# Kernel tuning notes

Hardware: AMD Instinct MI355X
Metric: run time of the kernel (lower is better)

## Reference

```python
import jax, jax.numpy as jnp
import numpy as np

LN_EPS = 1e-5
TOP_K = 2


def setup_inputs() -> dict:
    key = jax.random.key(0)
    ks = jax.random.split(key, 6)
    B, S, D, I, E = 4, 1024, 1024, 4096, 8
    return {
        "hidden_states": jax.random.normal(ks[0], (B, S, D), dtype=jnp.float32),
        "attention_mask": jnp.ones((B, S), dtype=jnp.float32),
        "gate_w": jax.random.normal(ks[1], (E, D), dtype=jnp.float32) * 0.02,
        "w1": jax.random.normal(ks[2], (E, D, I), dtype=jnp.float32) * 0.02,
        "b1": jnp.zeros((E, I), dtype=jnp.float32),
        "w2": jax.random.normal(ks[3], (E, I, D), dtype=jnp.float32) * 0.02,
        "b2": jnp.zeros((E, D), dtype=jnp.float32),
        "ln_gamma": jnp.ones((D,), dtype=jnp.float32),
        "ln_beta": jnp.zeros((D,), dtype=jnp.float32),
    }


def reference(hidden_states, attention_mask, gate_w, w1, b1, w2, b2, ln_gamma, ln_beta):
    B, S, D = hidden_states.shape
    E = gate_w.shape[0]
    h = hidden_states.reshape(-1, D).astype(jnp.float32)  # (T, D)

    # --- gate: softmax over experts, top-2, renormalize ---
    logits = h @ gate_w.T                                  # (T, E)
    probs = jax.nn.softmax(logits, axis=-1)
    rw, sel = jax.lax.top_k(probs, TOP_K)                  # (T, k), (T, k)
    rw = rw / jnp.sum(rw, axis=-1, keepdims=True)

    # per-token dense combine weights: (T, E), zero for non-selected experts
    onehot = jax.nn.one_hot(sel, E, dtype=rw.dtype)        # (T, k, E)
    w_te = jnp.einsum('tk,tke->te', rw, onehot)            # (T, E)

    # --- expert FFNs (dense over all experts; weights zero-out non-selected) ---
    mid = jax.nn.gelu(jnp.einsum('td,edi->eti', h, w1) + b1[:, None, :], approximate=False)
    eout = jnp.einsum('eti,eid->etd', mid, w2) + b2[:, None, :]  # (E, T, D)
    moe_out = jnp.einsum('etd,te->td', eout, w_te)         # (T, D)

    out = moe_out.reshape(B, S, D) * attention_mask[..., None]
    out = hidden_states + out

    # LayerNorm
    mu = jnp.mean(out, axis=-1, keepdims=True)
    var = jnp.var(out, axis=-1, keepdims=True)
    out = (out - mu) * jax.lax.rsqrt(var + LN_EPS) * ln_gamma + ln_beta

    # load balancing loss: mse(expert_usage, uniform)
    T = h.shape[0]
    usage = jnp.sum(onehot, axis=(0, 1)) / T               # (E,)
    aux_loss = jnp.mean((usage - 1.0 / E) ** 2)
    return out, aux_loss
```

## Files before the change

### kernel.cpp

```cpp
#include <hip/hip_runtime.h>
#include <hip/hip_bf16.h>
#include <math.h>

#define T_TOK 4096
#define D_DIM 1024
#define I_DIM 4096
#define E_EXP 8
#define MAX_TILES 48

typedef __attribute__((ext_vector_type(8))) short bf16x8;
typedef __attribute__((ext_vector_type(4))) float f32x4;

__device__ __forceinline__ unsigned short f2bf(float x) {
    unsigned int u = __float_as_uint(x);
    u += 0x7fffu + ((u >> 16) & 1u);
    return (unsigned short)(u >> 16);
}

__device__ __forceinline__ void glds16(const unsigned short* g, unsigned short* l) {
    __builtin_amdgcn_global_load_lds(
        (const __attribute__((address_space(1))) unsigned int*)g,
        (__attribute__((address_space(3))) unsigned int*)(unsigned int)(unsigned long long)(void*)l,
        16, 0, 0);
}

#define VMWAIT4 asm volatile("s_waitcnt vmcnt(4)" ::: "memory")
#define VMWAIT3 asm volatile("s_waitcnt vmcnt(3)" ::: "memory")
#define VMWAIT0 asm volatile("s_waitcnt vmcnt(0)" ::: "memory")

__device__ __forceinline__ void bar() {
    asm volatile("" ::: "memory");
    __builtin_amdgcn_s_barrier();
    asm volatile("" ::: "memory");
}

__global__ void gate_kernel(const float* __restrict__ h, const float* __restrict__ gw,
                            int* __restrict__ counts, int* __restrict__ sel,
                            float* __restrict__ wgt) {
    int t = blockIdx.x;
    int tid = threadIdx.x;
    float acc[E_EXP];
#pragma unroll
    for (int e = 0; e < E_EXP; e++) acc[e] = 0.f;
    const float* hr = h + (size_t)t * D_DIM;
    for (int d = tid; d < D_DIM; d += 256) {
        float hv = hr[d];
#pragma unroll
        for (int e = 0; e < E_EXP; e++) acc[e] += hv * gw[e * D_DIM + d];
    }
#pragma unroll
    for (int e = 0; e < E_EXP; e++)
        for (int off = 32; off > 0; off >>= 1) acc[e] += __shfl_down(acc[e], off, 64);
    __shared__ float red[4][E_EXP];
    int wave = tid >> 6, lane = tid & 63;
    if (lane == 0) {
#pragma unroll
        for (int e = 0; e < E_EXP; e++) red[wave][e] = acc[e];
    }
    __syncthreads();
    if (tid == 0) {
        float lg[E_EXP];
#pragma unroll
        for (int e = 0; e < E_EXP; e++) lg[e] = red[0][e] + red[1][e] + red[2][e] + red[3][e];
        float mx = lg[0];
#pragma unroll
        for (int e = 1; e < E_EXP; e++) mx = fmaxf(mx, lg[e]);
        float p[E_EXP];
#pragma unroll
        for (int e = 0; e < E_EXP; e++) p[e] = expf(lg[e] - mx);
        int i0 = 0; float b0 = p[0];
#pragma unroll
        for (int e = 1; e < E_EXP; e++) if (p[e] > b0) { b0 = p[e]; i0 = e; }
        int i1 = -1; float b1v = -1.f;
#pragma unroll
        for (int e = 0; e < E_EXP; e++) if (e != i0 && p[e] > b1v) { b1v = p[e]; i1 = e; }
        float den = b0 + b1v;
        sel[2 * t] = i0; sel[2 * t + 1] = i1;
        wgt[2 * t] = b0 / den; wgt[2 * t + 1] = b1v / den;
        atomicAdd(&counts[i0], 1);
        atomicAdd(&counts[i1], 1);
    }
}

__global__ void offsets_kernel(const int* __restrict__ counts, int* __restrict__ offs,
                               int* __restrict__ cursors, float* __restrict__ aux_out,
                               int* __restrict__ tile_e, int* __restrict__ tile_m,
                               int* __restrict__ ntiles) {
    if (blockIdx.x == 0 && threadIdx.x == 0) {
        int off = 0; float aux = 0.f; int nt = 0;
        for (int e = 0; e < E_EXP; e++) {
            offs[e] = off; off += counts[e]; cursors[e] = 0;
            float u = (float)counts[e] / (float)T_TOK;
            float d = u - 1.0f / (float)E_EXP;
            aux += d * d;
            for (int m0 = 0; m0 < counts[e]; m0 += 256) {
                tile_e[nt] = e; tile_m[nt] = m0; nt++;
            }
        }
        ntiles[0] = nt;
        aux_out[0] = aux / (float)E_EXP;
    }
}

__global__ void scatter_kernel(const int* __restrict__ sel, const float* __restrict__ wgt,
                               const int* __restrict__ offs, int* __restrict__ cursors,
                               int* __restrict__ tok_list, float* __restrict__ tok_w,
                               int* __restrict__ slot_of) {
    int t = blockIdx.x * 256 + threadIdx.x;
    if (t >= T_TOK) return;
#pragma unroll
    for (int k = 0; k < 2; k++) {
        int e = sel[2 * t + k];
        int pos = atomicAdd(&cursors[e], 1);
        int idx = offs[e] + pos;
        tok_list[idx] = t;
        tok_w[idx] = wgt[2 * t + k];
        slot_of[2 * t + k] = idx;
    }
}

__global__ void cvtH_kernel(const float* __restrict__ src, unsigned short* __restrict__ dst) {
    size_t i = ((size_t)blockIdx.x * 256 + threadIdx.x) * 8;
    float4 a = *(const float4*)(src + i);
    float4 b = *(const float4*)(src + i + 4);
    union { unsigned short u[8]; uint4 v; } o;
    o.u[0] = f2bf(a.x); o.u[1] = f2bf(a.y); o.u[2] = f2bf(a.z); o.u[3] = f2bf(a.w);
    o.u[4] = f2bf(b.x); o.u[5] = f2bf(b.y); o.u[6] = f2bf(b.z); o.u[7] = f2bf(b.w);
    *(uint4*)(dst + i) = o.v;
}

__global__ void transpose_cvt_kernel(const float* __restrict__ src, unsigned short* __restrict__ dst,
                                     int R, int C) {
    __shared__ float tile[32][33];
    int e = blockIdx.z;
    const float* s = src + (size_t)e * R * C;
    unsigned short* d = dst + (size_t)e * R * C;
    int c0 = blockIdx.x * 32, r0 = blockIdx.y * 32;
    int tx = threadIdx.x, ty = threadIdx.y;
#pragma unroll
    for (int j = 0; j < 4; j++)
        tile[ty + 8 * j][tx] = s[(size_t)(r0 + ty + 8 * j) * C + c0 + tx];
    __syncthreads();
#pragma unroll
    for (int j = 0; j < 4; j++)
        d[(size_t)(c0 + ty + 8 * j) * R + r0 + tx] = f2bf(tile[tx][ty + 8 * j]);
}

template <int MODE>
__launch_bounds__(512, 2)
__global__ void moe_gemm_kernel(const unsigned short* __restrict__ Abase,
                                const unsigned short* __restrict__ Bt,
                                const float* __restrict__ bias,
                                const int* __restrict__ counts, const int* __restrict__ offs,
                                const int* __restrict__ tile_e, const int* __restrict__ tile_m,
                                const int* __restrict__ ntiles,
                                const int* __restrict__ tok_list, const float* __restrict__ tok_w,
                                unsigned short* __restrict__ midout, float* __restrict__ slotbuf) {
    constexpr int K  = (MODE == 0) ? D_DIM : I_DIM;
    constexpr int N  = (MODE == 0) ? I_DIM : D_DIM;
    constexpr int BN = (MODE == 0) ? 256 : 128;
    constexpr int NJ = BN / 64;
    constexpr int SB = BN / 128;
    constexpr int NT = K / 32;

    __shared__ __align__(16) unsigned short lA[4][256 * 32];
    __shared__ __align__(16) unsigned short lB[4][BN * 32];

    const int nwg  = gridDim.x * gridDim.y;
    const int flat = blockIdx.y * gridDim.x + blockIdx.x;
    const int q8 = nwg >> 3, r8 = nwg & 7;
    const int xcd = flat & 7, pos = flat >> 3;
    const int id2 = (xcd < r8 ? xcd * (q8 + 1) : r8 * (q8 + 1) + (xcd - r8) * q8) + pos;
    const int tix = id2 / gridDim.y;
    const int nb  = id2 % gridDim.y;
    if (tix >= ntiles[0]) return;

    const int e   = tile_e[tix];
    const int m0  = tile_m[tix];
    const int Ne  = counts[e];
    const int seg = offs[e];
    const int n0  = nb * BN;

    const int tid  = threadIdx.x;
    const int w    = tid >> 6;
    const int lane = tid & 63;
    const int quad = lane >> 4;
    const int l15  = lane & 15;
    const int wm   = (w >> 2) * 128;
    const int wn   = (w & 3) * (NJ * 16);

    const int lrow = lane >> 2;
    const int lcol = (lane & 3) * 8;
    const unsigned short* gA0;
    const unsigned short* gA1;
    {
        int mr0 = m0 + w * 32 + lrow;
        int mr1 = mr0 + 16;
        int c0 = (mr0 < Ne) ? mr0 : 0;
        int c1 = (mr1 < Ne) ? mr1 : 0;
        size_t r0, r1;
        if (MODE == 0) { r0 = (size_t)tok_list[seg + c0] * K; r1 = (size_t)tok_list[seg + c1] * K; }
        else           { r0 = (size_t)(seg + c0) * K;         r1 = (size_t)(seg + c1) * K; }
        gA0 = Abase + r0 + lcol;
        gA1 = Abase + r1 + lcol;
    }
    const unsigned short* Bte = Bt + (size_t)e * N * K;
    const unsigned short* gB0 = Bte + (size_t)(n0 + w * (16 * SB) + lrow) * K + lcol;
    const unsigned short* gB1 = gB0 + (size_t)16 * K;

    auto ISSUE = [&](int kt2) {
        const int b2  = kt2 & 3;
        const int off = kt2 * 32;
        glds16(gA0 + off, &lA[b2][w * 1024]);
        glds16(gA1 + off, &lA[b2][w * 1024 + 512]);
        glds16(gB0 + off, &lB[b2][w * (SB * 512)]);
        if constexpr (MODE == 0) glds16(gB1 + off, &lB[b2][w * 1024 + 512]);
    };

    f32x4 acc[8][NJ];
#pragma unroll
    for (int a = 0; a < 8; a++)
#pragma unroll
        for (int j = 0; j < NJ; j++) acc[a][j] = (f32x4){0.f, 0.f, 0.f, 0.f};

    const int sc = quad * 8;

    auto TILE = [&](int kt2) {
        const unsigned short* LA = lA[kt2 & 3];
        const unsigned short* LB = lB[kt2 & 3];
        bf16x8 bv[NJ];
#pragma unroll
        for (int j = 0; j < NJ; j++)
            bv[j] = *(const bf16x8*)&LB[(wn + j * 16 + l15) * 32 + sc];
#pragma unroll
        for (int pm = 0; pm < 2; pm++) {
            bf16x8 av[4];
#pragma unroll
            for (int ii = 0; ii < 4; ii++)
                av[ii] = *(const bf16x8*)&LA[(wm + pm * 64 + ii * 16 + l15) * 32 + sc];
            __builtin_amdgcn_s_setprio(1);
#pragma unroll
            for (int ii = 0; ii < 4; ii++)
#pragma unroll
                for (int j = 0; j < NJ; j++)
                    acc[pm * 4 + ii][j] = __builtin_amdgcn_mfma_f32_16x16x32_bf16(
                        av[ii], bv[j], acc[pm * 4 + ii][j], 0, 0, 0);
            __builtin_amdgcn_s_setprio(0);
        }
    };

    ISSUE(0);
    ISSUE(1);

    for (int kt = 0; kt < NT; kt += 2) {
        if constexpr (MODE == 0) { VMWAIT4; } else { VMWAIT3; }
        bar();
        if (kt + 2 < NT) ISSUE(kt + 2);
        TILE(kt);
        if (kt + 3 < NT) {
            if constexpr (MODE == 0) { VMWAIT4; } else { VMWAIT3; }
        } else {
            VMWAIT0;
        }
        bar();
        if (kt + 3 < NT) ISSUE(kt + 3);
        TILE(kt + 1);
    }

    const float* be = bias + (size_t)e * N;
#pragma unroll
    for (int a = 0; a < 8; a++) {
        const int mbase = m0 + wm + (a >> 2) * 64 + (a & 3) * 16 + quad * 4;
#pragma unroll
        for (int j = 0; j < NJ; j++) {
            const int n = n0 + wn + j * 16 + l15;
            const float bvl = be[n];
#pragma unroll
            for (int r = 0; r < 4; r++) {
                const int m = mbase + r;
                if (m < Ne) {
                    float v = acc[a][j][r] + bvl;
                    if (MODE == 0) {
                        v = 0.5f * v * (1.0f + erff(v * 0.70710678118654752f));
                        midout[(size_t)(seg + m) * N + n] = f2bf(v);
                    } else {
                        slotbuf[(size_t)(seg + m) * N + n] = tok_w[seg + m] * v;
                    }
                }
            }
        }
    }
}

__global__ void ln_kernel(const float* __restrict__ hs, const float* __restrict__ mask,
                          const float* __restrict__ slotbuf, const int* __restrict__ slot_of,
                          const float* __restrict__ gamma, const float* __restrict__ beta,
                          float* __restrict__ outp) {
    int t = blockIdx.x, tid = threadIdx.x;
    int s0 = slot_of[2 * t], s1 = slot_of[2 * t + 1];
    float mk = mask[t];
    const float4* hr = (const float4*)(hs + (size_t)t * D_DIM);
    const float4* p0 = (const float4*)(slotbuf + (size_t)s0 * D_DIM);
    const float4* p1 = (const float4*)(slotbuf + (size_t)s1 * D_DIM);
    float4 hv = hr[tid], a = p0[tid], b = p1[tid];
    float x0 = hv.x + mk * (a.x + b.x);
    float x1 = hv.y + mk * (a.y + b.y);
    float x2 = hv.z + mk * (a.z + b.z);
    float x3 = hv.w + mk * (a.w + b.w);
    float sum = x0 + x1 + x2 + x3;
    float sq = x0 * x0 + x1 * x1 + x2 * x2 + x3 * x3;
    for (int off = 32; off > 0; off >>= 1) {
        sum += __shfl_down(sum, off, 64);
        sq += __shfl_down(sq, off, 64);
    }
    __shared__ float rsum[4], rsq[4];
    __shared__ float mu_s, rstd_s;
    int wave = tid >> 6, lane = tid & 63;
    if (lane == 0) { rsum[wave] = sum; rsq[wave] = sq; }
    __syncthreads();
    if (tid == 0) {
        float s = rsum[0] + rsum[1] + rsum[2] + rsum[3];
        float q = rsq[0] + rsq[1] + rsq[2] + rsq[3];
        float mu = s / (float)D_DIM;
        float var = q / (float)D_DIM - mu * mu;
        mu_s = mu; rstd_s = rsqrtf(var + 1e-5f);
    }
    __syncthreads();
    float mu = mu_s, rstd = rstd_s;
    const float4* g4 = (const float4*)gamma;
    const float4* b4 = (const float4*)beta;
    float4 g = g4[tid], bb = b4[tid];
    float4 o;
    o.x = (x0 - mu) * rstd * g.x + bb.x;
    o.y = (x1 - mu) * rstd * g.y + bb.y;
    o.z = (x2 - mu) * rstd * g.z + bb.z;
    o.w = (x3 - mu) * rstd * g.w + bb.w;
    ((float4*)(outp + (size_t)t * D_DIM))[tid] = o;
}

extern "C" void kernel_launch(void* const* d_in, const int* in_sizes, int n_in,
                              void* d_out, int out_size, void* d_ws, size_t ws_size,
                              hipStream_t stream) {
    const float* hs    = (const float*)d_in[0];
    const float* mask  = (const float*)d_in[1];
    const float* gw    = (const float*)d_in[2];
    const float* w1    = (const float*)d_in[3];
    const float* b1    = (const float*)d_in[4];
    const float* w2    = (const float*)d_in[5];
    const float* b2    = (const float*)d_in[6];
    const float* gamma = (const float*)d_in[7];
    const float* beta  = (const float*)d_in[8];
    float* out = (float*)d_out;

    char* ws = (char*)d_ws;
    int*   counts   = (int*)(ws + 0);
    int*   cursors  = (int*)(ws + 64);
    int*   offs     = (int*)(ws + 128);
    int*   ntiles   = (int*)(ws + 256);
    int*   tile_e   = (int*)(ws + 512);
    int*   tile_m   = (int*)(ws + 1024);
    int*   sel      = (int*)(ws + 4096);
    float* wgt      = (float*)(ws + 4096 + 1 * 32768);
    int*   slot_of  = (int*)(ws + 4096 + 2 * 32768);
    int*   tok_list = (int*)(ws + 4096 + 3 * 32768);
    float* tok_w    = (float*)(ws + 4096 + 4 * 32768);
    unsigned short* Hbf = (unsigned short*)(ws + (1ull << 20));
    unsigned short* W1t = (unsigned short*)(ws + (9ull << 20));
    unsigned short* W2t = (unsigned short*)(ws + (73ull << 20));
    unsigned short* mid = (unsigned short*)(ws + (137ull << 20));
    float* slotbuf      = (float*)(ws + (201ull << 20));

    hipMemsetAsync(counts, 0, 64, stream);
    gate_kernel<<<T_TOK, 256, 0, stream>>>(hs, gw, counts, sel, wgt);
    offsets_kernel<<<1, 64, 0, stream>>>(counts, offs, cursors, out + (size_t)T_TOK * D_DIM,
                                         tile_e, tile_m, ntiles);
    scatter_kernel<<<T_TOK / 256, 256, 0, stream>>>(sel, wgt, offs, cursors, tok_list, tok_w, slot_of);
    cvtH_kernel<<<(T_TOK * D_DIM / 8) / 256, 256, 0, stream>>>(hs, Hbf);
    transpose_cvt_kernel<<<dim3(I_DIM / 32, D_DIM / 32, E_EXP), dim3(32, 8), 0, stream>>>(w1, W1t, D_DIM, I_DIM);
    transpose_cvt_kernel<<<dim3(D_DIM / 32, I_DIM / 32, E_EXP), dim3(32, 8), 0, stream>>>(w2, W2t, I_DIM, D_DIM);
    moe_gemm_kernel<0><<<dim3(MAX_TILES, I_DIM / 256), 512, 0, stream>>>(
        Hbf, W1t, b1, counts, offs, tile_e, tile_m, ntiles, tok_list, tok_w, mid, nullptr);
    moe_gemm_kernel<1><<<dim3(MAX_TILES, D_DIM / 128), 512, 0, stream>>>(
        mid, W2t, b2, counts, offs, tile_e, tile_m, ntiles, tok_list, tok_w, nullptr, slotbuf);
    ln_kernel<<<T_TOK, 256, 0, stream>>>(hs, mask, slotbuf, slot_of, gamma, beta, out);
}
```

Before: 817.4 us.

## Restructure MoE GEMM pipeline with swizzled LDS, split A/B loads, uniform 256 N-tile

Rewrites the grouped GEMM main loop into a finer-grained schedule: A and B global-to-LDS loads are issued separately and interleaved between half-tile MFMA batches, with explicit lgkmcnt waits and barriers around each MFMA group. Adds an XOR swizzle on the LDS column offset to cut bank conflicts on fragment reads. The down-projection GEMM now uses a 256-wide N tile like the up-projection, and MAX_TILES shrinks from 48 to 40 to trim the grid. This brings more barriers per k-step, fewer workgroups for the second GEMM, and a tile cap that could be too small for unbalanced routing.

```diff
diff --git a/kernel.cpp b/kernel.cpp
--- a/kernel.cpp
+++ b/kernel.cpp
@@ -6,7 +6,7 @@
 #define D_DIM 1024
 #define I_DIM 4096
 #define E_EXP 8
-#define MAX_TILES 48
+#define MAX_TILES 40
 
 typedef __attribute__((ext_vector_type(8))) short bf16x8;
 typedef __attribute__((ext_vector_type(4))) float f32x4;
@@ -25,13 +25,11 @@
 }
 
 #define VMWAIT4 asm volatile("s_waitcnt vmcnt(4)" ::: "memory")
-#define VMWAIT3 asm volatile("s_waitcnt vmcnt(3)" ::: "memory")
 #define VMWAIT0 asm volatile("s_waitcnt vmcnt(0)" ::: "memory")
+#define LGKM0   asm volatile("s_waitcnt lgkmcnt(0)" ::: "memory")
 
 __device__ __forceinline__ void bar() {
-    asm volatile("" ::: "memory");
     __builtin_amdgcn_s_barrier();
-    asm volatile("" ::: "memory");
 }
 
 __global__ void gate_kernel(const float* __restrict__ h, const float* __restrict__ gw,
@@ -158,13 +156,10 @@
                                 unsigned short* __restrict__ midout, float* __restrict__ slotbuf) {
     constexpr int K  = (MODE == 0) ? D_DIM : I_DIM;
     constexpr int N  = (MODE == 0) ? I_DIM : D_DIM;
-    constexpr int BN = (MODE == 0) ? 256 : 128;
-    constexpr int NJ = BN / 64;
-    constexpr int SB = BN / 128;
     constexpr int NT = K / 32;
 
     __shared__ __align__(16) unsigned short lA[4][256 * 32];
-    __shared__ __align__(16) unsigned short lB[4][BN * 32];
+    __shared__ __align__(16) unsigned short lB[4][256 * 32];
 
     const int nwg  = gridDim.x * gridDim.y;
     const int flat = blockIdx.y * gridDim.x + blockIdx.x;
@@ -179,7 +174,7 @@
     const int m0  = tile_m[tix];
     const int Ne  = counts[e];
     const int seg = offs[e];
-    const int n0  = nb * BN;
+    const int n0  = nb * 256;
 
     const int tid  = threadIdx.x;
     const int w    = tid >> 6;
@@ -187,12 +182,13 @@
     const int quad = lane >> 4;
     const int l15  = lane & 15;
     const int wm   = (w >> 2) * 128;
-    const int wn   = (w & 3) * (NJ * 16);
+    const int wn   = (w & 3) * 64;
 
     const int lrow = lane >> 2;
-    const int lcol = (lane & 3) * 8;
-    const unsigned short* gA0;
-    const unsigned short* gA1;
+    const int scol = (((lane & 3) ^ ((lane >> 3) & 3)) & 3) * 8;
+    const int rs   = (((quad ^ ((l15 >> 1) & 3)) & 3) * 8);
+
+    const unsigned short *gA0, *gA1;
     {
         int mr0 = m0 + w * 32 + lrow;
         int mr1 = mr0 + 16;
@@ -201,70 +197,85 @@
         size_t r0, r1;
         if (MODE == 0) { r0 = (size_t)tok_list[seg + c0] * K; r1 = (size_t)tok_list[seg + c1] * K; }
         else           { r0 = (size_t)(seg + c0) * K;         r1 = (size_t)(seg + c1) * K; }
-        gA0 = Abase + r0 + lcol;
-        gA1 = Abase + r1 + lcol;
+        gA0 = Abase + r0 + scol;
+        gA1 = Abase + r1 + scol;
     }
     const unsigned short* Bte = Bt + (size_t)e * N * K;
-    const unsigned short* gB0 = Bte + (size_t)(n0 + w * (16 * SB) + lrow) * K + lcol;
+    const unsigned short* gB0 = Bte + (size_t)(n0 + w * 32 + lrow) * K + scol;
     const unsigned short* gB1 = gB0 + (size_t)16 * K;
 
-    auto ISSUE = [&](int kt2) {
-        const int b2  = kt2 & 3;
-        const int off = kt2 * 32;
-        glds16(gA0 + off, &lA[b2][w * 1024]);
-        glds16(gA1 + off, &lA[b2][w * 1024 + 512]);
-        glds16(gB0 + off, &lB[b2][w * (SB * 512)]);
-        if constexpr (MODE == 0) glds16(gB1 + off, &lB[b2][w * 1024 + 512]);
-    };
-
-    f32x4 acc[8][NJ];
+    auto ISSUE_A = [&](int t) {
+        const int b = t & 3, off = t * 32;
+        glds16(gA0 + off, &lA[b][w * 1024]);
+        glds16(gA1 + off, &lA[b][w * 1024 + 512]);
+    };
+    auto ISSUE_B = [&](int t) {
+        const int b = t & 3, off = t * 32;
+        glds16(gB0 + off, &lB[b][w * 1024]);
+        glds16(gB1 + off, &lB[b][w * 1024 + 512]);
+    };
+
+    f32x4 acc[8][4];
 #pragma unroll
     for (int a = 0; a < 8; a++)
 #pragma unroll
-        for (int j = 0; j < NJ; j++) acc[a][j] = (f32x4){0.f, 0.f, 0.f, 0.f};
-
-    const int sc = quad * 8;
-
-    auto TILE = [&](int kt2) {
-        const unsigned short* LA = lA[kt2 & 3];
-        const unsigned short* LB = lB[kt2 & 3];
-        bf16x8 bv[NJ];
-#pragma unroll
-        for (int j = 0; j < NJ; j++)
-            bv[j] = *(const bf16x8*)&LB[(wn + j * 16 + l15) * 32 + sc];
-#pragma unroll
-        for (int pm = 0; pm < 2; pm++) {
-            bf16x8 av[4];
-#pragma unroll
-            for (int ii = 0; ii < 4; ii++)
-                av[ii] = *(const bf16x8*)&LA[(wm + pm * 64 + ii * 16 + l15) * 32 + sc];
-            __builtin_amdgcn_s_setprio(1);
-#pragma unroll
-            for (int ii = 0; ii < 4; ii++)
-#pragma unroll
-                for (int j = 0; j < NJ; j++)
-                    acc[pm * 4 + ii][j] = __builtin_amdgcn_mfma_f32_16x16x32_bf16(
-                        av[ii], bv[j], acc[pm * 4 + ii][j], 0, 0, 0);
-            __builtin_amdgcn_s_setprio(0);
-        }
-    };
-
-    ISSUE(0);
-    ISSUE(1);
-
-    for (int kt = 0; kt < NT; kt += 2) {
-        if constexpr (MODE == 0) { VMWAIT4; } else { VMWAIT3; }
-        bar();
-        if (kt + 2 < NT) ISSUE(kt + 2);
-        TILE(kt);
-        if (kt + 3 < NT) {
-            if constexpr (MODE == 0) { VMWAIT4; } else { VMWAIT3; }
-        } else {
-            VMWAIT0;
-        }
-        bar();
-        if (kt + 3 < NT) ISSUE(kt + 3);
-        TILE(kt + 1);
+        for (int j = 0; j < 4; j++) acc[a][j] = (f32x4){0.f, 0.f, 0.f, 0.f};
+
+    bf16x8 bv[4], av[4];
+    auto READ_BV = [&](int t) {
+        const unsigned short* LB = lB[t & 3];
+#pragma unroll
+        for (int j = 0; j < 4; j++)
+            bv[j] = *(const bf16x8*)&LB[(wn + j * 16 + l15) * 32 + rs];
+    };
+    auto READ_AV = [&](int t, int pm) {
+        const unsigned short* LA = lA[t & 3];
+#pragma unroll
+        for (int ii = 0; ii < 4; ii++)
+            av[ii] = *(const bf16x8*)&LA[(wm + pm * 64 + ii * 16 + l15) * 32 + rs];
+    };
+    auto MFMA16 = [&](int pm) {
+        __builtin_amdgcn_s_setprio(1);
+#pragma unroll
+        for (int ii = 0; ii < 4; ii++)
+#pragma unroll
+            for (int j = 0; j < 4; j++)
+                acc[pm * 4 + ii][j] = __builtin_amdgcn_mfma_f32_16x16x32_bf16(
+                    av[ii], bv[j], acc[pm * 4 + ii][j], 0, 0, 0);
+        __builtin_amdgcn_s_setprio(0);
+    };
+
+    ISSUE_A(0); ISSUE_B(0);
+    ISSUE_A(1); ISSUE_B(1);
+    VMWAIT4;
+    bar();
+
+    for (int kt = 0; kt < NT - 2; kt += 2) {
+        READ_BV(kt); READ_AV(kt, 0);
+        ISSUE_A(kt + 2);
+        bar(); LGKM0; MFMA16(0); bar();
+        READ_AV(kt, 1);
+        ISSUE_B(kt + 2);
+        VMWAIT4;
+        bar(); LGKM0; MFMA16(1); bar();
+        READ_BV(kt + 1); READ_AV(kt + 1, 0);
+        ISSUE_A(kt + 3);
+        bar(); LGKM0; MFMA16(0); bar();
+        READ_AV(kt + 1, 1);
+        ISSUE_B(kt + 3);
+        VMWAIT4;
+        bar(); LGKM0; MFMA16(1); bar();
+    }
+    {
+        READ_BV(NT - 2); READ_AV(NT - 2, 0);
+        bar(); LGKM0; MFMA16(0); bar();
+        READ_AV(NT - 2, 1);
+        VMWAIT0;
+        bar(); LGKM0; MFMA16(1); bar();
+        READ_BV(NT - 1); READ_AV(NT - 1, 0);
+        bar(); LGKM0; MFMA16(0); bar();
+        READ_AV(NT - 1, 1);
+        LGKM0; MFMA16(1);
     }
 
     const float* be = bias + (size_t)e * N;
@@ -272,7 +283,7 @@
     for (int a = 0; a < 8; a++) {
         const int mbase = m0 + wm + (a >> 2) * 64 + (a & 3) * 16 + quad * 4;
 #pragma unroll
-        for (int j = 0; j < NJ; j++) {
+        for (int j = 0; j < 4; j++) {
             const int n = n0 + wn + j * 16 + l15;
             const float bvl = be[n];
 #pragma unroll
@@ -380,7 +391,7 @@
     transpose_cvt_kernel<<<dim3(D_DIM / 32, I_DIM / 32, E_EXP), dim3(32, 8), 0, stream>>>(w2, W2t, I_DIM, D_DIM);
     moe_gemm_kernel<0><<<dim3(MAX_TILES, I_DIM / 256), 512, 0, stream>>>(
         Hbf, W1t, b1, counts, offs, tile_e, tile_m, ntiles, tok_list, tok_w, mid, nullptr);
-    moe_gemm_kernel<1><<<dim3(MAX_TILES, D_DIM / 128), 512, 0, stream>>>(
+    moe_gemm_kernel<1><<<dim3(MAX_TILES, D_DIM / 256), 512, 0, stream>>>(
         mid, W2t, b2, counts, offs, tile_e, tile_m, ntiles, tok_list, tok_w, nullptr, slotbuf);
     ln_kernel<<<T_TOK, 256, 0, stream>>>(hs, mask, slotbuf, slot_of, gamma, beta, out);
 }
```

After: 777.2 us. 1.05x faster.
